# Optimization experiments

Measured on AMD Instinct MI355X. Metric: run time of the kernel, lower is better.

## Reference

```python
import jax, jax.numpy as jnp
import numpy as np

EPS = 0.3
LAYERS = 2


def setup_inputs() -> dict:
    key = jax.random.key(0)
    ks = jax.random.split(key, 8)
    N, F, H, C, E = 50000, 512, 128, 40, 800000

    def xavier(k, shape):
        fan_out, fan_in = shape[0], shape[-1]
        std = 1.414 * np.sqrt(2.0 / (fan_in + fan_out))
        return (jax.random.normal(k, shape, jnp.float32) * std).astype(jnp.float32)

    return {
        "x": jax.random.normal(ks[0], (N, F), jnp.float32),
        "t1_w": xavier(ks[1], (H, F)),
        "t1_b": jnp.zeros((H,), jnp.float32),
        "t2_w": xavier(ks[2], (C, H)),
        "t2_b": jnp.zeros((C,), jnp.float32),
        "gate_w": xavier(ks[3], (LAYERS, 2 * H)),  # Linear(2H,1) weight per layer
        "gate_b": jnp.zeros((LAYERS,), jnp.float32),
        "edge_index": jax.random.randint(ks[4], (2, E), 0, N, jnp.int32),
    }


def reference(x, t1_w, t1_b, t2_w, t2_b, gate_w, gate_b, edge_index):
    N = x.shape[0]
    H = t1_w.shape[0]
    row, col = edge_index[0], edge_index[1]  # source, target

    # norm_degree = degree(row).clamp(min=1) ** -0.5
    deg = jax.ops.segment_sum(jnp.ones_like(row, dtype=x.dtype), row, num_segments=N)
    nd = jnp.clip(deg, 1.0) ** -0.5  # [N]
    nd_r, nd_c = nd[row], nd[col]    # [E]

    # dropout is identity in eval mode
    h = jax.nn.relu(x @ t1_w.T + t1_b)  # [N,H]
    raw = h
    for l in range(LAYERS):
        h_src = h[row]  # x_j, [E,H]
        h_dst = h[col]  # [E,H]
        # gate(cat([h[row], h[col]])) == h_src @ W[:H] + h_dst @ W[H:] + b
        g = jnp.tanh(h_src @ gate_w[l, :H] + h_dst @ gate_w[l, H:] + gate_b[l])  # [E]
        norm = g * nd_r * nd_c  # [E]
        agg = jax.ops.segment_sum(norm[:, None] * h_src, col, num_segments=N)  # scatter-add at targets
        h = EPS * raw + agg
    out = h @ t2_w.T + t2_b  # [N,C]
    return jax.nn.log_softmax(out, axis=1)
```

## Files before the change

### kernel.cpp

```cpp
#include <hip/hip_runtime.h>
#include <math.h>

#define F_DIM 512
#define H_DIM 128
#define C_DIM 40
#define EPS_F 0.3f
#define NBLK 256

typedef float f32x4 __attribute__((ext_vector_type(4)));
typedef unsigned int u32x4 __attribute__((ext_vector_type(4)));
typedef __bf16 bf16x8 __attribute__((ext_vector_type(8)));
typedef unsigned short ushort_t;
typedef unsigned char uchar_t;

__device__ inline float bflo(unsigned t) { return __builtin_bit_cast(float, t << 16); }
__device__ inline float bfhi(unsigned t) { return __builtin_bit_cast(float, t & 0xffff0000u); }
__device__ inline unsigned short f2bf(float f) {
  unsigned u = __builtin_bit_cast(unsigned, f);
  u = (u + 0x7fffu + ((u >> 16) & 1u)) >> 16;
  return (unsigned short)u;
}
__device__ inline unsigned pack2bf(float a, float b) {
  unsigned ua = __builtin_bit_cast(unsigned, a);
  unsigned ub = __builtin_bit_cast(unsigned, b);
  ua = (ua + 0x7fffu + ((ua >> 16) & 1u)) >> 16;
  ub = (ub + 0x7fffu + ((ub >> 16) & 1u)) >> 16;
  return ua | (ub << 16);
}
__device__ inline float fast_tanh(float x) {
  float e = __expf(2.0f * x);
  return 1.0f - 2.0f / (e + 1.0f);
}
#define RL(x, k)  __builtin_amdgcn_readlane((x), (k))
#define RLF(x, k) __builtin_bit_cast(float, __builtin_amdgcn_readlane(__builtin_bit_cast(int, (x)), (k)))


__global__ __launch_bounds__(256) void part_count(const int* __restrict__ row,
    const int* __restrict__ col, int* __restrict__ blkhist, int E, int nbkt, int chunk) {
  __shared__ int ch[256], rh[256];
  int t = threadIdx.x, b = blockIdx.x;
  ch[t] = 0; rh[t] = 0;
  __syncthreads();
  int s = b * chunk, e = min(E, s + chunk);
  for (int i = s + t; i < e; i += 256) {
    atomicAdd(&ch[((unsigned)col[i]) >> 8], 1);
    atomicAdd(&rh[((unsigned)row[i]) >> 8], 1);
  }
  __syncthreads();
  if (t < nbkt) {
    blkhist[t * NBLK + b] = ch[t];
    blkhist[(nbkt + t) * NBLK + b] = rh[t];
  }
}

__global__ __launch_bounds__(256) void part_scatter(const int* __restrict__ row,
    const int* __restrict__ col, const int* __restrict__ blkhist,
    int* __restrict__ bktbase, unsigned* __restrict__ colpart,
    uchar_t* __restrict__ rowpart, int E, int nbkt, int chunk) {
  __shared__ int sbase[400];
  __shared__ int stot[400];
  __shared__ int psum[256];
  __shared__ int sc[400];
  __shared__ int coff[400];
  int t = threadIdx.x, b = blockIdx.x;
  int nrows = 2 * nbkt;
  for (int rr = t; rr < nrows; rr += 256) {
    const int* rp = &blkhist[rr * NBLK];
    int pre = 0, tot = 0;
    for (int i = 0; i < NBLK; ++i) {
      int v = rp[i];
      pre += (i < b) ? v : 0;
      tot += v;
    }
    sbase[rr] = pre; stot[rr] = tot;
  }
  __syncthreads();
  int e0 = (2 * t     < nrows) ? stot[2 * t]     : 0;
  int e1 = (2 * t + 1 < nrows) ? stot[2 * t + 1] : 0;
  psum[t] = e0 + e1;
  __syncthreads();
  for (int off = 1; off < 256; off <<= 1) {
    int add = (t >= off) ? psum[t - off] : 0;
    __syncthreads();
    psum[t] += add;
    __syncthreads();
  }
  int pex = (t == 0) ? 0 : psum[t - 1];
  if (2 * t < nrows)     sc[2 * t]     = pex + sbase[2 * t];
  if (2 * t + 1 < nrows) sc[2 * t + 1] = pex + e0 + sbase[2 * t + 1];
  if (b == 0) {
    if (2 * t < nrows)     bktbase[2 * t]     = pex;
    if (2 * t + 1 < nrows) bktbase[2 * t + 1] = pex + e0;
    if (t == 0) bktbase[nrows] = 2 * E;
  }
  for (int rr = t; rr < nrows; rr += 256) coff[rr] = 0;
  __syncthreads();
  int s = b * chunk, e = min(E, s + chunk);
  for (int i = s + t; i < e; i += 256) {
    unsigned c = (unsigned)col[i], r = (unsigned)row[i];
    int bc = (int)(c >> 8), br = (int)(r >> 8);
    int pc = sc[bc] + atomicAdd(&coff[bc], 1);
    colpart[pc] = (r << 8) | (c & 255u);
    int pr = sc[nbkt + br] + atomicAdd(&coff[nbkt + br], 1) - E;
    rowpart[pr] = (uchar_t)(r & 255u);
  }
}

__global__ __launch_bounds__(256) void bucket_both(const unsigned* __restrict__ colpart,
    const uchar_t* __restrict__ rowpart, const int* __restrict__ bktbase,
    int* __restrict__ col_ptr, int* __restrict__ csr_src, ushort_t* __restrict__ tgt,
    float* __restrict__ nd, int N, int E, int nbkt) {
  __shared__ int cnt[256], ex[256], off[256];
  int t = threadIdx.x, bb = blockIdx.x;
  if (bb < nbkt) {
    int bkt = bb;
    int s = bktbase[bkt], e = bktbase[bkt + 1];
    cnt[t] = 0; off[t] = 0;
    __syncthreads();
    for (int i = s + t; i < e; i += 256)
      atomicAdd(&cnt[(int)(colpart[i] & 255u)], 1);
    __syncthreads();
    ex[t] = cnt[t];
    __syncthreads();
    for (int o = 1; o < 256; o <<= 1) {
      int v = (t >= o) ? ex[t - o] : 0;
      __syncthreads();
      ex[t] += v;
      __syncthreads();
    }
    int excl = (t == 0) ? 0 : ex[t - 1];
    __syncthreads();
    ex[t] = excl;
    __syncthreads();
    int node = bkt * 256 + t;
    if (node < N) col_ptr[node] = s + ex[t];
    if (bkt == 0 && t == 0) col_ptr[N] = E;
    for (int i = s + t; i < e; i += 256) {
      unsigned p = colpart[i];
      int lb = (int)(p & 255u);
      int dst = s + ex[lb] + atomicAdd(&off[lb], 1);
      csr_src[dst] = (int)(p >> 8);
      tgt[dst] = (ushort_t)(bkt * 256 + lb);
    }
  } else {
    int bkt = bb - nbkt;
    int s = bktbase[nbkt + bkt] - E, e = bktbase[nbkt + bkt + 1] - E;
    cnt[t] = 0;
    __syncthreads();
    for (int i = s + t; i < e; i += 256)
      atomicAdd(&cnt[(int)rowpart[i]], 1);
    __syncthreads();
    int node = bkt * 256 + t;
    if (node < N) {
      int d = cnt[t] < 1 ? 1 : cnt[t];
      nd[node] = 1.0f / sqrtf((float)d);
    }
  }
}


__global__ __launch_bounds__(256) void gemm1_mfma(const float* __restrict__ x,
    const float* __restrict__ w, const float* __restrict__ b,
    const float* __restrict__ gwl, const float* __restrict__ gb,
    const float* __restrict__ nd,
    ushort_t* __restrict__ hbf, float2* __restrict__ pack0,
    float* __restrict__ s2a, int N) {
  __shared__ u32x4 AsBuf[1024];
  __shared__ u32x4 BsBuf[1024];
  char* Asc = (char*)AsBuf;
  char* Bsc = (char*)BsBuf;

  int t = threadIdx.x;
  int lane = t & 63;
  int wid = t >> 6;
  int wm = wid >> 1;
  int wn = wid & 1;
  int m0 = blockIdx.x * 128;
  int ql = lane & 15;

  f32x4 acc[4][4];
#pragma unroll
  for (int i = 0; i < 4; ++i)
#pragma unroll
    for (int j = 0; j < 4; ++j) acc[i][j] = (f32x4){0.f, 0.f, 0.f, 0.f};

  float bias[4], g1v[4], g2v[4];
#pragma unroll
  for (int j = 0; j < 4; ++j) {
    int c = wn * 64 + j * 16 + ql;
    bias[j] = b[c];
    g1v[j] = gwl[c];
    g2v[j] = gwl[H_DIM + c];
  }

  for (int kk = 0; kk < F_DIM; kk += 64) {
#pragma unroll
    for (int q = 0; q < 4; ++q) {
      int c = q * 256 + t;
      int row = c >> 3, kc = c & 7;
      int gm = m0 + row;
      f32x4 v0 = {0.f, 0.f, 0.f, 0.f}, v1 = {0.f, 0.f, 0.f, 0.f};
      if (gm < N) {
        const float* src = &x[(size_t)gm * F_DIM + kk + kc * 8];
        v0 = *(const f32x4*)src;
        v1 = *(const f32x4*)(src + 4);
      }
      u32x4 pk;
      pk[0] = pack2bf(v0[0], v0[1]);
      pk[1] = pack2bf(v0[2], v0[3]);
      pk[2] = pack2bf(v1[0], v1[1]);
      pk[3] = pack2bf(v1[2], v1[3]);
      *(u32x4*)(Asc + row * 128 + ((kc ^ (row & 7)) << 4)) = pk;
    }
#pragma unroll
    for (int q = 0; q < 4; ++q) {
      int c = q * 256 + t;
      int row = c >> 3, kc = c & 7;
      const float* src = &w[(size_t)row * F_DIM + kk + kc * 8];
      f32x4 v0 = *(const f32x4*)src;
      f32x4 v1 = *(const f32x4*)(src + 4);
      u32x4 pk;
      pk[0] = pack2bf(v0[0], v0[1]);
      pk[1] = pack2bf(v0[2], v0[3]);
      pk[2] = pack2bf(v1[0], v1[1]);
      pk[3] = pack2bf(v1[2], v1[3]);
      *(u32x4*)(Bsc + row * 128 + ((kc ^ (row & 7)) << 4)) = pk;
    }
    __syncthreads();
#pragma unroll
    for (int kh = 0; kh < 2; ++kh) {
      bf16x8 af[4], bfr[4];
      int kc = kh * 4 + (lane >> 4);
#pragma unroll
      for (int i = 0; i < 4; ++i) {
        int row = wm * 64 + i * 16 + ql;
        af[i] = *(const bf16x8*)(Asc + row * 128 + ((kc ^ (row & 7)) << 4));
      }
#pragma unroll
      for (int j = 0; j < 4; ++j) {
        int row = wn * 64 + j * 16 + ql;
        bfr[j] = *(const bf16x8*)(Bsc + row * 128 + ((kc ^ (row & 7)) << 4));
      }
#pragma unroll
      for (int i = 0; i < 4; ++i)
#pragma unroll
        for (int j = 0; j < 4; ++j)
          acc[i][j] = __builtin_amdgcn_mfma_f32_16x16x32_bf16(af[i], bfr[j], acc[i][j], 0, 0, 0);
    }
    __syncthreads();
  }

  float gp1[4][4], gp2[4][4];
#pragma unroll
  for (int i = 0; i < 4; ++i)
#pragma unroll
    for (int r = 0; r < 4; ++r) { gp1[i][r] = 0.f; gp2[i][r] = 0.f; }

#pragma unroll
  for (int i = 0; i < 4; ++i) {
    int rbase = m0 + wm * 64 + i * 16 + ((lane >> 4) * 4);
#pragma unroll
    for (int j = 0; j < 4; ++j) {
      int col = wn * 64 + j * 16 + ql;
#pragma unroll
      for (int r = 0; r < 4; ++r) {
        int gr = rbase + r;
        float o = fmaxf(acc[i][j][r] + bias[j], 0.f);
        if (gr < N) hbf[(size_t)gr * H_DIM + col] = f2bf(o);
        gp1[i][r] = fmaf(o, g1v[j], gp1[i][r]);
        gp2[i][r] = fmaf(o, g2v[j], gp2[i][r]);
      }
    }
  }
#pragma unroll
  for (int i = 0; i < 4; ++i)
#pragma unroll
    for (int r = 0; r < 4; ++r) {
#pragma unroll
      for (int m = 1; m < 16; m <<= 1) {
        gp1[i][r] += __shfl_xor(gp1[i][r], m);
        gp2[i][r] += __shfl_xor(gp2[i][r], m);
      }
    }
  float* pgA = (float*)AsBuf;
  float* pgB = (float*)AsBuf + 256;
  if (ql == 0) {
#pragma unroll
    for (int i = 0; i < 4; ++i)
#pragma unroll
      for (int r = 0; r < 4; ++r) {
        int lr = wm * 64 + i * 16 + (lane >> 4) * 4 + r;
        pgA[lr * 2 + wn] = gp1[i][r];
        pgB[lr * 2 + wn] = gp2[i][r];
      }
  }
  __syncthreads();
  if (t < 128) {
    int gr = m0 + t;
    if (gr < N) {
      float p1 = pgA[t * 2] + pgA[t * 2 + 1];
      float p2 = pgB[t * 2] + pgB[t * 2 + 1];
      float ndv = nd[gr];
      pack0[gr] = make_float2(p1, ndv);
      s2a[gr] = p2 + gb[0];
    }
  }
}


__global__ __launch_bounds__(256) void coef_kernel(const int* __restrict__ csr_src,
    const ushort_t* __restrict__ tgt, const float2* __restrict__ pack,
    const float* __restrict__ s2pb, const float* __restrict__ ndarr,
    float* __restrict__ coef, int E) {
  int i = blockIdx.x * 256 + threadIdx.x;
  if (i >= E) return;
  int u = csr_src[i];
  int v = (int)tgt[i];
  float2 pk = pack[u];
  coef[i] = fast_tanh(pk.x + s2pb[v]) * pk.y * ndarr[v];
}


#define GBODY(K)                                                               \
  {                                                                            \
    int u_##K = RL(u, j + K);                                                  \
    const ushort_t* r_##K = HSRC_ + (size_t)u_##K * H_DIM;                     \
    tv[K] = *(const unsigned*)(r_##K + lane * 2);                              \
  }

#define AGG_CORE(HSRC)                                                         \
  float ax = 0.f, ay = 0.f;                                                    \
  {                                                                            \
    const ushort_t* HSRC_ = (HSRC);                                            \
    int p0 = col_ptr[v], p1v = col_ptr[v + 1];                                 \
    for (int base = p0; base < p1v; base += 64) {                              \
      int idx = base + lane;                                                   \
      int u = 0;                                                               \
      float cf = 0.f;                                                          \
      if (idx < p1v) {                                                         \
        u = csr_src[idx];                                                      \
        cf = coef[idx];                                                        \
      }                                                                        \
      int cnt = p1v - base;                                                    \
      if (cnt > 64) cnt = 64;                                                  \
      int j = 0;                                                               \
      for (; j + 8 <= cnt; j += 8) {                                           \
        unsigned tv[8];                                                        \
        GBODY(0) GBODY(1) GBODY(2) GBODY(3)                                    \
        GBODY(4) GBODY(5) GBODY(6) GBODY(7)                                    \
        float c0 = RLF(cf, j + 0), c1 = RLF(cf, j + 1);                        \
        float c2 = RLF(cf, j + 2), c3 = RLF(cf, j + 3);                        \
        float c4 = RLF(cf, j + 4), c5 = RLF(cf, j + 5);                        \
        float c6 = RLF(cf, j + 6), c7 = RLF(cf, j + 7);                        \
        ax = fmaf(c0, bflo(tv[0]), ax); ay = fmaf(c0, bfhi(tv[0]), ay);        \
        ax = fmaf(c1, bflo(tv[1]), ax); ay = fmaf(c1, bfhi(tv[1]), ay);        \
        ax = fmaf(c2, bflo(tv[2]), ax); ay = fmaf(c2, bfhi(tv[2]), ay);        \
        ax = fmaf(c3, bflo(tv[3]), ax); ay = fmaf(c3, bfhi(tv[3]), ay);        \
        ax = fmaf(c4, bflo(tv[4]), ax); ay = fmaf(c4, bfhi(tv[4]), ay);        \
        ax = fmaf(c5, bflo(tv[5]), ax); ay = fmaf(c5, bfhi(tv[5]), ay);        \
        ax = fmaf(c6, bflo(tv[6]), ax); ay = fmaf(c6, bfhi(tv[6]), ay);        \
        ax = fmaf(c7, bflo(tv[7]), ax); ay = fmaf(c7, bfhi(tv[7]), ay);        \
      }                                                                        \
      for (; j + 4 <= cnt; j += 4) {                                           \
        unsigned tv[4];                                                        \
        GBODY(0) GBODY(1) GBODY(2) GBODY(3)                                    \
        float c0 = RLF(cf, j + 0), c1 = RLF(cf, j + 1);                        \
        float c2 = RLF(cf, j + 2), c3 = RLF(cf, j + 3);                        \
        ax = fmaf(c0, bflo(tv[0]), ax); ay = fmaf(c0, bfhi(tv[0]), ay);        \
        ax = fmaf(c1, bflo(tv[1]), ax); ay = fmaf(c1, bfhi(tv[1]), ay);        \
        ax = fmaf(c2, bflo(tv[2]), ax); ay = fmaf(c2, bfhi(tv[2]), ay);        \
        ax = fmaf(c3, bflo(tv[3]), ax); ay = fmaf(c3, bfhi(tv[3]), ay);        \
      }                                                                        \
      for (; j < cnt; ++j) {                                                   \
        int uj = RL(u, j);                                                     \
        float cj = RLF(cf, j);                                                 \
        unsigned tj = *(const unsigned*)(HSRC_ + (size_t)uj * H_DIM + lane * 2);\
        ax = fmaf(cj, bflo(tj), ax); ay = fmaf(cj, bfhi(tj), ay);              \
      }                                                                        \
    }                                                                          \
  }

__global__ __launch_bounds__(256) void agg1(const ushort_t* __restrict__ hbf,
    const float* __restrict__ coef, const int* __restrict__ col_ptr,
    const int* __restrict__ csr_src, const float* __restrict__ nd,
    ushort_t* __restrict__ houtbf,
    const float* __restrict__ gwl, const float* __restrict__ gb1,
    float2* __restrict__ packo, float* __restrict__ s2o, int N) {
  int t = threadIdx.x;
  int v = blockIdx.x * 4 + (t >> 6);
  int lane = t & 63;
  if (v >= N) return;
  unsigned rv = *(const unsigned*)&hbf[(size_t)v * H_DIM + lane * 2];
  AGG_CORE(hbf)
  float ox = fmaf(EPS_F, bflo(rv), ax);
  float oy = fmaf(EPS_F, bfhi(rv), ay);
  *(unsigned*)&houtbf[(size_t)v * H_DIM + lane * 2] = pack2bf(ox, oy);
  float2 g1 = *(const float2*)&gwl[lane * 2];
  float2 g2 = *(const float2*)&gwl[H_DIM + lane * 2];
  float q1 = ox * g1.x + oy * g1.y;
  float q2 = ox * g2.x + oy * g2.y;
#pragma unroll
  for (int off = 32; off > 0; off >>= 1) {
    q1 += __shfl_xor(q1, off);
    q2 += __shfl_xor(q2, off);
  }
  if (lane == 0) {
    packo[v] = make_float2(q1, nd[v]);
    s2o[v] = q2 + gb1[0];
  }
}

__global__ __launch_bounds__(256) void agg2(const ushort_t* __restrict__ hbf,
    const ushort_t* __restrict__ rawbf, const float* __restrict__ coef,
    const int* __restrict__ col_ptr, const int* __restrict__ csr_src,
    const float* __restrict__ w2, const float* __restrict__ b2,
    float* __restrict__ out, int N) {
  __shared__ float ws[C_DIM][129];
  __shared__ float bsh[C_DIM];
  __shared__ float hsm[4][H_DIM];
  int t = threadIdx.x;
  for (int i = t; i < C_DIM * H_DIM; i += 256) ws[i / H_DIM][i % H_DIM] = w2[i];
  if (t < C_DIM) bsh[t] = b2[t];
  __syncthreads();
  int wave = t >> 6, lane = t & 63;
  int v = blockIdx.x * 4 + wave;
  bool act = v < N;
  if (act) {
    unsigned rv = *(const unsigned*)&rawbf[(size_t)v * H_DIM + lane * 2];
    AGG_CORE(hbf)
    float ox = fmaf(EPS_F, bflo(rv), ax);
    float oy = fmaf(EPS_F, bfhi(rv), ay);
    hsm[wave][lane * 2] = ox;
    hsm[wave][lane * 2 + 1] = oy;
  }
  __syncthreads();
  float accv = 0.f;
  if (act && lane < C_DIM) {
#pragma unroll 8
    for (int k = 0; k < H_DIM; ++k)
      accv = fmaf(hsm[wave][k], ws[lane][k], accv);
    accv += bsh[lane];
  }
  float m = (lane < C_DIM) ? accv : -1e30f;
#pragma unroll
  for (int off = 32; off > 0; off >>= 1) m = fmaxf(m, __shfl_xor(m, off));
  float ex = (lane < C_DIM) ? expf(accv - m) : 0.f;
  float s = ex;
#pragma unroll
  for (int off = 32; off > 0; off >>= 1) s += __shfl_xor(s, off);
  float lse = m + logf(s);
  if (act && lane < C_DIM) out[(size_t)v * C_DIM + lane] = accv - lse;
}


extern "C" void kernel_launch(void* const* d_in, const int* in_sizes, int n_in,
                              void* d_out, int out_size, void* d_ws, size_t ws_size,
                              hipStream_t stream) {
  const float* x   = (const float*)d_in[0];
  const float* t1w = (const float*)d_in[1];
  const float* t1b = (const float*)d_in[2];
  const float* t2w = (const float*)d_in[3];
  const float* t2b = (const float*)d_in[4];
  const float* gw  = (const float*)d_in[5];
  const float* gb  = (const float*)d_in[6];
  const int*   ei  = (const int*)d_in[7];
  const int N = in_sizes[0] / F_DIM;
  const int E = in_sizes[7] / 2;
  float* out = (float*)d_out;

  char* p = (char*)d_ws;
  auto take = [&](size_t bytes) {
    char* r = p;
    p += (bytes + 255) & ~(size_t)255;
    return r;
  };
  ushort_t* h0 = (ushort_t*)take((size_t)N * H_DIM * 2);
  ushort_t* h1 = (ushort_t*)take((size_t)N * H_DIM * 2);
  float2* pack0 = (float2*)take((size_t)N * 8);
  float2* pack1 = (float2*)take((size_t)N * 8);
  float* s2a = (float*)take((size_t)N * 4);
  float* s2b = (float*)take((size_t)N * 4);
  float* nd  = (float*)take((size_t)N * 4);
  int* col_ptr = (int*)take((size_t)(N + 1) * 4);
  int* csr_src = (int*)take((size_t)E * 4);
  ushort_t* tgt = (ushort_t*)take((size_t)E * 2);
  float* coef = (float*)take((size_t)E * 4);

  const int nbkt = (N + 255) >> 8;
  const int chunk = (E + NBLK - 1) / NBLK;

  int* blkhist = (int*)take((size_t)2 * nbkt * NBLK * 4);
  int* bktbase = (int*)take((size_t)(2 * nbkt + 1) * 4);
  unsigned* colpart = (unsigned*)take((size_t)E * 4);
  uchar_t* rowpart  = (uchar_t*)take((size_t)E);

  const int* row = ei;
  const int* col = ei + E;

  part_count<<<NBLK, 256, 0, stream>>>(row, col, blkhist, E, nbkt, chunk);
  part_scatter<<<NBLK, 256, 0, stream>>>(row, col, blkhist, bktbase, colpart, rowpart, E, nbkt, chunk);
  bucket_both<<<2 * nbkt, 256, 0, stream>>>(colpart, rowpart, bktbase, col_ptr, csr_src, tgt, nd, N, E, nbkt);

  gemm1_mfma<<<(N + 127) / 128, 256, 0, stream>>>(x, t1w, t1b, gw, gb, nd, h0, pack0, s2a, N);

  int ebl = (E + 255) / 256;
  int nwb = (N + 3) / 4;
  coef_kernel<<<ebl, 256, 0, stream>>>(csr_src, tgt, pack0, s2a, nd, coef, E);
  agg1<<<nwb, 256, 0, stream>>>(h0, coef, col_ptr, csr_src, nd, h1,
                                gw + 2 * H_DIM, gb + 1, pack1, s2b, N);
  coef_kernel<<<ebl, 256, 0, stream>>>(csr_src, tgt, pack1, s2b, nd, coef, E);
  agg2<<<nwb, 256, 0, stream>>>(h1, h0, coef, col_ptr, csr_src,
                                t2w, t2b, out, N);
}
```

Measured before the change: 195.2 us.

## Split aggregation into column-quarter gather kernels and unfuse gate and output GEMM

The aggregation is restructured so that each block handles one 64-byte quarter of the feature columns, and each wave's lanes gather 4 edges at once, with shuffle-broadcast of indices and a cross-group reduction at the end. The gate projection and the final linear plus log-softmax move into separate kernels, gate_s and a grid-stride gemm2_lsm. The intent is better gather locality through narrower row segments and a wider spread of blocks. The cost is four times as many blocks re-reading CSR indices and coefficients, an extra h2 buffer and extra kernel launches.

```diff
diff --git a/kernel.cpp b/kernel.cpp
--- a/kernel.cpp
+++ b/kernel.cpp
@@ -31,8 +31,6 @@
   float e = __expf(2.0f * x);
   return 1.0f - 2.0f / (e + 1.0f);
 }
-#define RL(x, k)  __builtin_amdgcn_readlane((x), (k))
-#define RLF(x, k) __builtin_bit_cast(float, __builtin_amdgcn_readlane(__builtin_bit_cast(int, (x)), (k)))
 
 
 __global__ __launch_bounds__(256) void part_count(const int* __restrict__ row,
@@ -308,6 +306,31 @@
 }
 
 
+__global__ __launch_bounds__(256) void gate_s(const ushort_t* __restrict__ hbf,
+    const float* __restrict__ gwl, const float* __restrict__ gb1,
+    const float* __restrict__ nd, float2* __restrict__ packo,
+    float* __restrict__ s2o, int N) {
+  int wid = (blockIdx.x * 256 + threadIdx.x) >> 6;
+  int lane = threadIdx.x & 63;
+  if (wid >= N) return;
+  unsigned tv = *(const unsigned*)&hbf[(size_t)wid * H_DIM + lane * 2];
+  float hx = bflo(tv), hy = bfhi(tv);
+  float2 g1 = *(const float2*)&gwl[lane * 2];
+  float2 g2 = *(const float2*)&gwl[H_DIM + lane * 2];
+  float p1 = hx * g1.x + hy * g1.y;
+  float p2 = hx * g2.x + hy * g2.y;
+#pragma unroll
+  for (int off = 32; off > 0; off >>= 1) {
+    p1 += __shfl_xor(p1, off);
+    p2 += __shfl_xor(p2, off);
+  }
+  if (lane == 0) {
+    packo[wid] = make_float2(p1, nd[wid]);
+    s2o[wid] = p2 + gb1[0];
+  }
+}
+
+
 __global__ __launch_bounds__(256) void coef_kernel(const int* __restrict__ csr_src,
     const ushort_t* __restrict__ tgt, const float2* __restrict__ pack,
     const float* __restrict__ s2pb, const float* __restrict__ ndarr,
@@ -321,135 +344,114 @@
 }
 
 
-#define GBODY(K)                                                               \
-  {                                                                            \
-    int u_##K = RL(u, j + K);                                                  \
-    const ushort_t* r_##K = HSRC_ + (size_t)u_##K * H_DIM;                     \
-    tv[K] = *(const unsigned*)(r_##K + lane * 2);                              \
-  }
-
-#define AGG_CORE(HSRC)                                                         \
-  float ax = 0.f, ay = 0.f;                                                    \
-  {                                                                            \
-    const ushort_t* HSRC_ = (HSRC);                                            \
-    int p0 = col_ptr[v], p1v = col_ptr[v + 1];                                 \
-    for (int base = p0; base < p1v; base += 64) {                              \
-      int idx = base + lane;                                                   \
-      int u = 0;                                                               \
-      float cf = 0.f;                                                          \
-      if (idx < p1v) {                                                         \
-        u = csr_src[idx];                                                      \
-        cf = coef[idx];                                                        \
-      }                                                                        \
-      int cnt = p1v - base;                                                    \
-      if (cnt > 64) cnt = 64;                                                  \
-      int j = 0;                                                               \
-      for (; j + 8 <= cnt; j += 8) {                                           \
-        unsigned tv[8];                                                        \
-        GBODY(0) GBODY(1) GBODY(2) GBODY(3)                                    \
-        GBODY(4) GBODY(5) GBODY(6) GBODY(7)                                    \
-        float c0 = RLF(cf, j + 0), c1 = RLF(cf, j + 1);                        \
-        float c2 = RLF(cf, j + 2), c3 = RLF(cf, j + 3);                        \
-        float c4 = RLF(cf, j + 4), c5 = RLF(cf, j + 5);                        \
-        float c6 = RLF(cf, j + 6), c7 = RLF(cf, j + 7);                        \
-        ax = fmaf(c0, bflo(tv[0]), ax); ay = fmaf(c0, bfhi(tv[0]), ay);        \
-        ax = fmaf(c1, bflo(tv[1]), ax); ay = fmaf(c1, bfhi(tv[1]), ay);        \
-        ax = fmaf(c2, bflo(tv[2]), ax); ay = fmaf(c2, bfhi(tv[2]), ay);        \
-        ax = fmaf(c3, bflo(tv[3]), ax); ay = fmaf(c3, bfhi(tv[3]), ay);        \
-        ax = fmaf(c4, bflo(tv[4]), ax); ay = fmaf(c4, bfhi(tv[4]), ay);        \
-        ax = fmaf(c5, bflo(tv[5]), ax); ay = fmaf(c5, bfhi(tv[5]), ay);        \
-        ax = fmaf(c6, bflo(tv[6]), ax); ay = fmaf(c6, bfhi(tv[6]), ay);        \
-        ax = fmaf(c7, bflo(tv[7]), ax); ay = fmaf(c7, bfhi(tv[7]), ay);        \
-      }                                                                        \
-      for (; j + 4 <= cnt; j += 4) {                                           \
-        unsigned tv[4];                                                        \
-        GBODY(0) GBODY(1) GBODY(2) GBODY(3)                                    \
-        float c0 = RLF(cf, j + 0), c1 = RLF(cf, j + 1);                        \
-        float c2 = RLF(cf, j + 2), c3 = RLF(cf, j + 3);                        \
-        ax = fmaf(c0, bflo(tv[0]), ax); ay = fmaf(c0, bfhi(tv[0]), ay);        \
-        ax = fmaf(c1, bflo(tv[1]), ax); ay = fmaf(c1, bfhi(tv[1]), ay);        \
-        ax = fmaf(c2, bflo(tv[2]), ax); ay = fmaf(c2, bfhi(tv[2]), ay);        \
-        ax = fmaf(c3, bflo(tv[3]), ax); ay = fmaf(c3, bfhi(tv[3]), ay);        \
-      }                                                                        \
-      for (; j < cnt; ++j) {                                                   \
-        int uj = RL(u, j);                                                     \
-        float cj = RLF(cf, j);                                                 \
-        unsigned tj = *(const unsigned*)(HSRC_ + (size_t)uj * H_DIM + lane * 2);\
-        ax = fmaf(cj, bflo(tj), ax); ay = fmaf(cj, bfhi(tj), ay);              \
-      }                                                                        \
-    }                                                                          \
-  }
-
-__global__ __launch_bounds__(256) void agg1(const ushort_t* __restrict__ hbf,
-    const float* __restrict__ coef, const int* __restrict__ col_ptr,
-    const int* __restrict__ csr_src, const float* __restrict__ nd,
-    ushort_t* __restrict__ houtbf,
-    const float* __restrict__ gwl, const float* __restrict__ gb1,
-    float2* __restrict__ packo, float* __restrict__ s2o, int N) {
+__global__ __launch_bounds__(256) void agg_q(const ushort_t* __restrict__ hsrc,
+    const ushort_t* __restrict__ raw, const float* __restrict__ coef,
+    const int* __restrict__ col_ptr, const int* __restrict__ csr_src,
+    ushort_t* __restrict__ hout, int N) {
   int t = threadIdx.x;
-  int v = blockIdx.x * 4 + (t >> 6);
-  int lane = t & 63;
+  int wave = t >> 6, lane = t & 63;
+  int bid = blockIdx.x;
+  int q = (bid & 7) >> 1;
+  int half = bid & 1;
+  int v = (bid >> 3) * 8 + half * 4 + wave;
   if (v >= N) return;
-  unsigned rv = *(const unsigned*)&hbf[(size_t)v * H_DIM + lane * 2];
-  AGG_CORE(hbf)
-  float ox = fmaf(EPS_F, bflo(rv), ax);
-  float oy = fmaf(EPS_F, bfhi(rv), ay);
-  *(unsigned*)&houtbf[(size_t)v * H_DIM + lane * 2] = pack2bf(ox, oy);
-  float2 g1 = *(const float2*)&gwl[lane * 2];
-  float2 g2 = *(const float2*)&gwl[H_DIM + lane * 2];
-  float q1 = ox * g1.x + oy * g1.y;
-  float q2 = ox * g2.x + oy * g2.y;
-#pragma unroll
-  for (int off = 32; off > 0; off >>= 1) {
-    q1 += __shfl_xor(q1, off);
-    q2 += __shfl_xor(q2, off);
-  }
-  if (lane == 0) {
-    packo[v] = make_float2(q1, nd[v]);
-    s2o[v] = q2 + gb1[0];
-  }
-}
-
-__global__ __launch_bounds__(256) void agg2(const ushort_t* __restrict__ hbf,
-    const ushort_t* __restrict__ rawbf, const float* __restrict__ coef,
-    const int* __restrict__ col_ptr, const int* __restrict__ csr_src,
-    const float* __restrict__ w2, const float* __restrict__ b2,
+  int g = lane >> 4, qi = lane & 15;
+  int coloff = q * 64 + qi * 4;
+  const char* hq = (const char*)hsrc + coloff;
+  int p0 = col_ptr[v], p1v = col_ptr[v + 1];
+  float ax = 0.f, ay = 0.f;
+  for (int base = p0; base < p1v; base += 64) {
+    int idx = base + lane;
+    int u = 0;
+    float cf = 0.f;
+    if (idx < p1v) {
+      u = csr_src[idx];
+      cf = coef[idx];
+    }
+    int cnt = p1v - base;
+    if (cnt > 64) cnt = 64;
+    int j = 0;
+    for (; j + 16 <= cnt; j += 16) {
+      int u0 = __shfl(u, j + g);
+      int u1 = __shfl(u, j + 4 + g);
+      int u2 = __shfl(u, j + 8 + g);
+      int u3 = __shfl(u, j + 12 + g);
+      unsigned t0 = *(const unsigned*)(hq + (size_t)u0 * 256);
+      unsigned t1 = *(const unsigned*)(hq + (size_t)u1 * 256);
+      unsigned t2 = *(const unsigned*)(hq + (size_t)u2 * 256);
+      unsigned t3 = *(const unsigned*)(hq + (size_t)u3 * 256);
+      float c0 = __shfl(cf, j + g);
+      float c1 = __shfl(cf, j + 4 + g);
+      float c2 = __shfl(cf, j + 8 + g);
+      float c3 = __shfl(cf, j + 12 + g);
+      ax = fmaf(c0, bflo(t0), ax); ay = fmaf(c0, bfhi(t0), ay);
+      ax = fmaf(c1, bflo(t1), ax); ay = fmaf(c1, bfhi(t1), ay);
+      ax = fmaf(c2, bflo(t2), ax); ay = fmaf(c2, bfhi(t2), ay);
+      ax = fmaf(c3, bflo(t3), ax); ay = fmaf(c3, bfhi(t3), ay);
+    }
+    for (; j + 4 <= cnt; j += 4) {
+      int u0 = __shfl(u, j + g);
+      unsigned t0 = *(const unsigned*)(hq + (size_t)u0 * 256);
+      float c0 = __shfl(cf, j + g);
+      ax = fmaf(c0, bflo(t0), ax); ay = fmaf(c0, bfhi(t0), ay);
+    }
+    if (j < cnt) {
+      int e = j + g;
+      int ec = e < cnt ? e : cnt - 1;
+      int u0 = __shfl(u, ec);
+      float c0 = __shfl(cf, ec);
+      if (e >= cnt) c0 = 0.f;
+      unsigned t0 = *(const unsigned*)(hq + (size_t)u0 * 256);
+      ax = fmaf(c0, bflo(t0), ax); ay = fmaf(c0, bfhi(t0), ay);
+    }
+  }
+  ax += __shfl_xor(ax, 16); ax += __shfl_xor(ax, 32);
+  ay += __shfl_xor(ay, 16); ay += __shfl_xor(ay, 32);
+  if (g == 0) {
+    unsigned rv = *(const unsigned*)((const char*)raw + (size_t)v * 256 + coloff);
+    float ox = fmaf(EPS_F, bflo(rv), ax);
+    float oy = fmaf(EPS_F, bfhi(rv), ay);
+    *(unsigned*)((char*)hout + (size_t)v * 256 + coloff) = pack2bf(ox, oy);
+  }
+}
+
+
+__global__ __launch_bounds__(256) void gemm2_lsm(const ushort_t* __restrict__ hbf,
+    const float* __restrict__ w, const float* __restrict__ b,
     float* __restrict__ out, int N) {
   __shared__ float ws[C_DIM][129];
   __shared__ float bsh[C_DIM];
   __shared__ float hsm[4][H_DIM];
   int t = threadIdx.x;
-  for (int i = t; i < C_DIM * H_DIM; i += 256) ws[i / H_DIM][i % H_DIM] = w2[i];
-  if (t < C_DIM) bsh[t] = b2[t];
+  for (int i = t; i < C_DIM * H_DIM; i += 256) ws[i / H_DIM][i % H_DIM] = w[i];
+  if (t < C_DIM) bsh[t] = b[t];
   __syncthreads();
   int wave = t >> 6, lane = t & 63;
-  int v = blockIdx.x * 4 + wave;
-  bool act = v < N;
-  if (act) {
-    unsigned rv = *(const unsigned*)&rawbf[(size_t)v * H_DIM + lane * 2];
-    AGG_CORE(hbf)
-    float ox = fmaf(EPS_F, bflo(rv), ax);
-    float oy = fmaf(EPS_F, bfhi(rv), ay);
-    hsm[wave][lane * 2] = ox;
-    hsm[wave][lane * 2 + 1] = oy;
-  }
-  __syncthreads();
-  float accv = 0.f;
-  if (act && lane < C_DIM) {
+  for (int vb = blockIdx.x * 4; vb < N; vb += gridDim.x * 4) {
+    int v = vb + wave;
+    bool act = v < N;
+    if (act) {
+      unsigned hv = *(const unsigned*)&hbf[(size_t)v * H_DIM + lane * 2];
+      hsm[wave][lane * 2] = bflo(hv);
+      hsm[wave][lane * 2 + 1] = bfhi(hv);
+    }
+    __syncthreads();
+    float acc = 0.f;
+    if (act && lane < C_DIM) {
 #pragma unroll 8
-    for (int k = 0; k < H_DIM; ++k)
-      accv = fmaf(hsm[wave][k], ws[lane][k], accv);
-    accv += bsh[lane];
-  }
-  float m = (lane < C_DIM) ? accv : -1e30f;
-#pragma unroll
-  for (int off = 32; off > 0; off >>= 1) m = fmaxf(m, __shfl_xor(m, off));
-  float ex = (lane < C_DIM) ? expf(accv - m) : 0.f;
-  float s = ex;
-#pragma unroll
-  for (int off = 32; off > 0; off >>= 1) s += __shfl_xor(s, off);
-  float lse = m + logf(s);
-  if (act && lane < C_DIM) out[(size_t)v * C_DIM + lane] = accv - lse;
+      for (int k = 0; k < H_DIM; ++k)
+        acc = fmaf(hsm[wave][k], ws[lane][k], acc);
+      acc += bsh[lane];
+    }
+    float m = (lane < C_DIM) ? acc : -1e30f;
+    for (int off = 32; off > 0; off >>= 1) m = fmaxf(m, __shfl_xor(m, off));
+    float ex = (lane < C_DIM) ? expf(acc - m) : 0.f;
+    float s = ex;
+    for (int off = 32; off > 0; off >>= 1) s += __shfl_xor(s, off);
+    float lse = m + logf(s);
+    if (act && lane < C_DIM) out[(size_t)v * C_DIM + lane] = acc - lse;
+    __syncthreads();
+  }
 }
 
 
@@ -476,6 +478,7 @@
   };
   ushort_t* h0 = (ushort_t*)take((size_t)N * H_DIM * 2);
   ushort_t* h1 = (ushort_t*)take((size_t)N * H_DIM * 2);
+  ushort_t* h2 = (ushort_t*)take((size_t)N * H_DIM * 2);
   float2* pack0 = (float2*)take((size_t)N * 8);
   float2* pack1 = (float2*)take((size_t)N * 8);
   float* s2a = (float*)take((size_t)N * 4);
@@ -505,10 +508,14 @@
 
   int ebl = (E + 255) / 256;
   int nwb = (N + 3) / 4;
+  int nqb = ((N + 7) / 8) * 8;
+
   coef_kernel<<<ebl, 256, 0, stream>>>(csr_src, tgt, pack0, s2a, nd, coef, E);
-  agg1<<<nwb, 256, 0, stream>>>(h0, coef, col_ptr, csr_src, nd, h1,
-                                gw + 2 * H_DIM, gb + 1, pack1, s2b, N);
+  agg_q<<<nqb, 256, 0, stream>>>(h0, h0, coef, col_ptr, csr_src, h1, N);
+
+  gate_s<<<nwb, 256, 0, stream>>>(h1, gw + 2 * H_DIM, gb + 1, nd, pack1, s2b, N);
   coef_kernel<<<ebl, 256, 0, stream>>>(csr_src, tgt, pack1, s2b, nd, coef, E);
-  agg2<<<nwb, 256, 0, stream>>>(h1, h0, coef, col_ptr, csr_src,
-                                t2w, t2b, out, N);
-}
+  agg_q<<<nqb, 256, 0, stream>>>(h1, h0, coef, col_ptr, csr_src, h2, N);
+
+  gemm2_lsm<<<1024, 256, 0, stream>>>(h2, t2w, t2b, out, N);
+}
```

Result: slower. 300.7 us (+54.1%).
